# Performance work log

Hardware: AMD Instinct MI355X
Metric: run time of the kernel (lower is better)

The kernel has to match this reference:

```python
import jax, jax.numpy as jnp
import numpy as np

SIGMA = 1.0  # config.sigma
C_NUM = 512  # config.c_num
C_MIN, C_MAX = -1.0, 1.0


def setup_inputs() -> dict:
    key = jax.random.key(0)
    k1, k2 = jax.random.split(key)
    data = jax.random.normal(k1, (8, 16, 64, 64), dtype=jnp.float32)
    # uniform init in [c_min, c_max], matching torch.nn.init.uniform_
    centers = jax.random.uniform(k2, (C_NUM, 1), dtype=jnp.float32,
                                 minval=C_MIN, maxval=C_MAX)
    return {"data": data, "centers": centers}


def reference(data, centers):
    b, c, h, w = data.shape
    x = data.reshape(-1)                     # [N], N = b*c*h*w
    cvec = centers.reshape(-1)               # [K]
    dist = (x[:, None] - cvec[None, :]) ** 2  # [N, K]
    phisoft = jax.nn.softmax(-SIGMA * dist, axis=-1)   # [N, K]
    symbols = jnp.argmin(dist, axis=-1)                 # [N] int
    softout = (phisoft @ cvec).reshape(b, c, h, w)
    hardout = cvec[symbols].reshape(b, c, h, w)
    zbar = softout + jax.lax.stop_gradient(hardout - softout)
    return zbar, softout, hardout, symbols.reshape(b, c, h, w)
```

## Files before the change

### kernel.cpp

```cpp
#include <hip/hip_runtime.h>
#include <math.h>

#define K_CENTERS 512
#define T_TAB 8192
#define XMIN_T (-6.0f)
#define XMAX_T (6.0f)
#define H_TAB ((XMAX_T - XMIN_T) / (float)T_TAB)
#define INV_H ((float)T_TAB / (XMAX_T - XMIN_T))
#define SORT_BLOCKS 8
#define TAB_THREADS ((T_TAB + 1) * 8)
#define TAB_BLOCKS ((TAB_THREADS + 255) / 256)

__global__ __launch_bounds__(256) void setup_k(const float* __restrict__ centers,
                                               float2* __restrict__ pair,
                                               float2* __restrict__ tab) {
    int t = threadIdx.x;
    int b = blockIdx.x;
    if (b < SORT_BLOCKS) {
        __shared__ float c[K_CENTERS];
        c[t] = centers[t];
        c[t + 256] = centers[t + 256];
        __syncthreads();
        int cidx = b * 64 + (t >> 2);
        int p = t & 3;
        float x = c[cidx];
        int rank = 0;
        int j0 = p * 128;
#pragma unroll 8
        for (int i = 0; i < 128; ++i) {
            int j = j0 + i;
            float cj = c[j];
            rank += (cj < x || (cj == x && j < cidx)) ? 1 : 0;
        }
        rank += __shfl_xor(rank, 1);
        rank += __shfl_xor(rank, 2);
        if (p == 0) pair[rank] = make_float2(x, (float)cidx);
    } else {
        int gid = (b - SORT_BLOCKS) * 256 + t;
        int n = gid >> 3;
        int s = gid & 7;
        if (n > T_TAB) return;
        float xn = XMIN_T + (float)n * H_TAB;
        float w = 0.f, wc = 0.f;
        int ic = 0;
        int k0 = s * 64;
#pragma unroll 8
        for (int q = 0; q < 64; ++q) {
            float cv = centers[k0 + q];
            float d = xn - cv;
            float e = __expf(-d * d);
            w += e;
            wc = fmaf(e, cv, wc);
            ic += (cv < xn) ? 1 : 0;
        }
        w  += __shfl_xor(w, 1);  wc += __shfl_xor(wc, 1);  ic += __shfl_xor(ic, 1);
        w  += __shfl_xor(w, 2);  wc += __shfl_xor(wc, 2);  ic += __shfl_xor(ic, 2);
        w  += __shfl_xor(w, 4);  wc += __shfl_xor(wc, 4);  ic += __shfl_xor(ic, 4);
        if (s == 0) tab[n] = make_float2(wc / w, (float)ic);
    }
}

__global__ __launch_bounds__(256) void quant_main_k(const float* __restrict__ data,
                                                    const float2* __restrict__ pair,
                                                    const float2* __restrict__ tab,
                                                    float* __restrict__ out, int N) {
    __shared__ float2 lsP[K_CENTERS];
    int t = threadIdx.x;
    lsP[t] = pair[t];
    lsP[t + 256] = pair[t + 256];
    __syncthreads();

    int base = (blockIdx.x * 256 + t) * 4;
    if (base >= N) return;

    float4 xv = *reinterpret_cast<const float4*>(data + base);
    float xs[4] = {xv.x, xv.y, xv.z, xv.w};
    float zb[4], so[4], sy[4];

#pragma unroll
    for (int e = 0; e < 4; ++e) {
        float x = xs[e];
        float u = (x - XMIN_T) * INV_H;
        int i0 = (int)floorf(u);
        i0 = min(max(i0, 0), T_TAB - 1);
        float frac = u - (float)i0;
        frac = fminf(fmaxf(frac, 0.f), 1.f);
        float2 r0 = tab[i0];
        float2 r1 = tab[i0 + 1];
        so[e] = fmaf(frac, r1.x - r0.x, r0.x);
        int jlo = max((int)r0.y - 3, 0);
        int jhi = min((int)r1.y + 2, K_CENTERS - 1);
        float bd2 = 3.4e38f;
        float bfo = 1.0e9f;
        float bc = 0.f;
        for (int j = jlo; j <= jhi; ++j) {
            float2 P = lsP[j];
            float d = x - P.x;
            float d2 = d * d;
            bool better = (d2 < bd2) || ((d2 == bd2) && (P.y < bfo));
            if (better) { bd2 = d2; bfo = P.y; bc = P.x; }
        }
        zb[e] = bc;
        sy[e] = bfo;
    }

    *reinterpret_cast<float4*>(out + base)         = make_float4(zb[0], zb[1], zb[2], zb[3]);
    *reinterpret_cast<float4*>(out + N + base)     = make_float4(so[0], so[1], so[2], so[3]);
    *reinterpret_cast<float4*>(out + 2 * N + base) = make_float4(zb[0], zb[1], zb[2], zb[3]);
    *reinterpret_cast<float4*>(out + 3 * N + base) = make_float4(sy[0], sy[1], sy[2], sy[3]);
}

extern "C" void kernel_launch(void* const* d_in, const int* in_sizes, int n_in,
                              void* d_out, int out_size, void* d_ws, size_t ws_size,
                              hipStream_t stream) {
    const float* data    = (const float*)d_in[0];
    const float* centers = (const float*)d_in[1];
    float* out = (float*)d_out;
    int N = in_sizes[0];

    float2* pair = (float2*)d_ws;
    float2* tab  = pair + K_CENTERS;

    setup_k<<<SORT_BLOCKS + TAB_BLOCKS, 256, 0, stream>>>(centers, pair, tab);

    int mainThreads = N / 4;
    quant_main_k<<<(mainThreads + 255) / 256, 256, 0, stream>>>(data, pair, tab, out, N);
}
```

Before: 16.39 us.

## Halve lookup table and stage it with sorted centers in LDS

Cuts the softmax lookup table from 8192 to 4096 entries, so the setup kernel needs half as many table blocks. The table and the sorted center pairs now sit in one contiguous workspace, and each main-kernel block copies both into shared memory with float4 loads, so table lookups hit LDS rather than global memory. The rank computation in the sort also reads centers as float4. The coarser table widens linear-interpolation error in the soft output, and each block now loads about 36KB of LDS, which may limit occupancy.

```diff
diff --git a/kernel.cpp b/kernel.cpp
--- a/kernel.cpp
+++ b/kernel.cpp
@@ -2,39 +2,44 @@
 #include <math.h>
 
 #define K_CENTERS 512
-#define T_TAB 8192
+#define T_TAB 4096
 #define XMIN_T (-6.0f)
 #define XMAX_T (6.0f)
 #define H_TAB ((XMAX_T - XMIN_T) / (float)T_TAB)
 #define INV_H ((float)T_TAB / (XMAX_T - XMIN_T))
 #define SORT_BLOCKS 8
-#define TAB_THREADS ((T_TAB + 1) * 8)
-#define TAB_BLOCKS ((TAB_THREADS + 255) / 256)
+#define TAB_BLOCKS (((T_TAB + 1) * 8 + 255) / 256)
+#define WS_PAIRS 512
+#define WS_TAB 4100
+#define WS_TOTAL (WS_PAIRS + WS_TAB)
 
 __global__ __launch_bounds__(256) void setup_k(const float* __restrict__ centers,
-                                               float2* __restrict__ pair,
-                                               float2* __restrict__ tab) {
+                                               float2* __restrict__ ws2) {
     int t = threadIdx.x;
     int b = blockIdx.x;
     if (b < SORT_BLOCKS) {
-        __shared__ float c[K_CENTERS];
+        __shared__ alignas(16) float c[K_CENTERS];
         c[t] = centers[t];
         c[t + 256] = centers[t + 256];
         __syncthreads();
         int cidx = b * 64 + (t >> 2);
         int p = t & 3;
         float x = c[cidx];
+        const float4* c4 = reinterpret_cast<const float4*>(c);
+        int q0 = p * 32;
         int rank = 0;
-        int j0 = p * 128;
 #pragma unroll 8
-        for (int i = 0; i < 128; ++i) {
-            int j = j0 + i;
-            float cj = c[j];
-            rank += (cj < x || (cj == x && j < cidx)) ? 1 : 0;
+        for (int i = 0; i < 32; ++i) {
+            float4 cj = c4[q0 + i];
+            int j = (q0 + i) * 4;
+            rank += (cj.x < x || (cj.x == x && (j + 0) < cidx)) ? 1 : 0;
+            rank += (cj.y < x || (cj.y == x && (j + 1) < cidx)) ? 1 : 0;
+            rank += (cj.z < x || (cj.z == x && (j + 2) < cidx)) ? 1 : 0;
+            rank += (cj.w < x || (cj.w == x && (j + 3) < cidx)) ? 1 : 0;
         }
         rank += __shfl_xor(rank, 1);
         rank += __shfl_xor(rank, 2);
-        if (p == 0) pair[rank] = make_float2(x, (float)cidx);
+        if (p == 0) ws2[rank] = make_float2(x, (float)cidx);
     } else {
         int gid = (b - SORT_BLOCKS) * 256 + t;
         int n = gid >> 3;
@@ -53,22 +58,27 @@
             wc = fmaf(e, cv, wc);
             ic += (cv < xn) ? 1 : 0;
         }
-        w  += __shfl_xor(w, 1);  wc += __shfl_xor(wc, 1);  ic += __shfl_xor(ic, 1);
-        w  += __shfl_xor(w, 2);  wc += __shfl_xor(wc, 2);  ic += __shfl_xor(ic, 2);
-        w  += __shfl_xor(w, 4);  wc += __shfl_xor(wc, 4);  ic += __shfl_xor(ic, 4);
-        if (s == 0) tab[n] = make_float2(wc / w, (float)ic);
+        w += __shfl_xor(w, 1); wc += __shfl_xor(wc, 1); ic += __shfl_xor(ic, 1);
+        w += __shfl_xor(w, 2); wc += __shfl_xor(wc, 2); ic += __shfl_xor(ic, 2);
+        w += __shfl_xor(w, 4); wc += __shfl_xor(wc, 4); ic += __shfl_xor(ic, 4);
+        if (s == 0) ws2[WS_PAIRS + n] = make_float2(wc / w, (float)ic);
     }
 }
 
 __global__ __launch_bounds__(256) void quant_main_k(const float* __restrict__ data,
-                                                    const float2* __restrict__ pair,
-                                                    const float2* __restrict__ tab,
+                                                    const float2* __restrict__ ws2,
                                                     float* __restrict__ out, int N) {
-    __shared__ float2 lsP[K_CENTERS];
+    __shared__ alignas(16) float2 buf[WS_TOTAL];
     int t = threadIdx.x;
-    lsP[t] = pair[t];
-    lsP[t + 256] = pair[t + 256];
+    {
+        const float4* src = reinterpret_cast<const float4*>(ws2);
+        float4* dst = reinterpret_cast<float4*>(buf);
+#pragma unroll
+        for (int i = t; i < WS_TOTAL / 2; i += 256) dst[i] = src[i];
+    }
     __syncthreads();
+    const float2* lsP  = buf;
+    const float2* tabL = buf + WS_PAIRS;
 
     int base = (blockIdx.x * 256 + t) * 4;
     if (base >= N) return;
@@ -85,8 +95,8 @@
         i0 = min(max(i0, 0), T_TAB - 1);
         float frac = u - (float)i0;
         frac = fminf(fmaxf(frac, 0.f), 1.f);
-        float2 r0 = tab[i0];
-        float2 r1 = tab[i0 + 1];
+        float2 r0 = tabL[i0];
+        float2 r1 = tabL[i0 + 1];
         so[e] = fmaf(frac, r1.x - r0.x, r0.x);
         int jlo = max((int)r0.y - 3, 0);
         int jhi = min((int)r1.y + 2, K_CENTERS - 1);
@@ -118,11 +128,10 @@
     float* out = (float*)d_out;
     int N = in_sizes[0];
 
-    float2* pair = (float2*)d_ws;
-    float2* tab  = pair + K_CENTERS;
+    float2* ws2 = (float2*)d_ws;
 
-    setup_k<<<SORT_BLOCKS + TAB_BLOCKS, 256, 0, stream>>>(centers, pair, tab);
+    setup_k<<<SORT_BLOCKS + TAB_BLOCKS, 256, 0, stream>>>(centers, ws2);
 
-    int mainThreads = N / 4;
-    quant_main_k<<<(mainThreads + 255) / 256, 256, 0, stream>>>(data, pair, tab, out, N);
+    int mainBlocks = (N / 4 + 255) / 256;
+    quant_main_k<<<mainBlocks, 256, 0, stream>>>(data, ws2, out, N);
 }
```

Result: slower. 18.09 us (+10.4%).
